# Performance work log

Measured on AMD Instinct MI355X. Metric: run time of the kernel, lower is better.

## Reference

```python
import jax, jax.numpy as jnp
import numpy as np

N_NODES = 50000
N_EDGES = 1_600_000
F_IN = 256
F_OUT = 256


def _gcn_conv(x, edge_index, W, b, num_nodes):
    """PyG GCNConv: add self-loops, symmetric deg^-1/2 normalization,
    linear transform, scatter-add aggregation, plus bias."""
    src, dst = edge_index[0], edge_index[1]
    loop = jnp.arange(num_nodes, dtype=src.dtype)
    src = jnp.concatenate([src, loop])  # [E+N]
    dst = jnp.concatenate([dst, loop])
    # degree of target nodes (edge_weight = 1), computed with self-loops
    deg = jax.ops.segment_sum(jnp.ones_like(dst, dtype=x.dtype), dst,
                              num_segments=num_nodes)
    dis = jnp.where(deg > 0, jax.lax.rsqrt(jnp.maximum(deg, 1.0)), 0.0)
    norm = dis[src] * dis[dst]  # [E+N]
    h = x @ W                   # [N, F_out]
    msg = h[src] * norm[:, None]                      # gather + scale
    out = jax.ops.segment_sum(msg, dst, num_segments=num_nodes)  # scatter-add
    return out + b


def setup_inputs() -> dict:
    key = jax.random.key(0)
    ks = jax.random.split(key, 6)
    x = jax.random.normal(ks[0], (N_NODES, F_IN), dtype=jnp.float32)
    edge_index = jax.random.randint(ks[1], (2, N_EDGES), 0, N_NODES,
                                    dtype=jnp.int64 if jax.config.jax_enable_x64 else jnp.int32)
    s = 1.0 / np.sqrt(F_IN)
    W1 = jax.random.normal(ks[2], (F_IN, F_OUT), dtype=jnp.float32) * s
    b1 = jnp.zeros((F_OUT,), dtype=jnp.float32)
    W2 = jax.random.normal(ks[3], (F_OUT, F_OUT), dtype=jnp.float32) * (1.0 / np.sqrt(F_OUT))
    b2 = jnp.zeros((F_OUT,), dtype=jnp.float32)
    prelu_a = jnp.full((F_OUT,), 0.25, dtype=jnp.float32)  # torch PReLU init
    return {"x": x, "edge_index": edge_index, "W1": W1, "b1": b1,
            "W2": W2, "b2": b2, "prelu_a": prelu_a}


def reference(x, edge_index, W1, b1, W2, b2, prelu_a):
    n = x.shape[0]
    z = _gcn_conv(x, edge_index, W1, b1, n)
    z = _gcn_conv(z, edge_index, W2, b2, n)
    # per-channel PReLU
    z = jnp.where(z >= 0, z, prelu_a[None, :] * z)
    return z
```

## Files before the change

kernel.cpp:

```cpp
#include <hip/hip_runtime.h>
#include <stdint.h>

typedef __attribute__((ext_vector_type(8))) short bf16x8;
typedef __attribute__((ext_vector_type(4))) float f32x4;
typedef __attribute__((ext_vector_type(4))) float float4v;
typedef __attribute__((ext_vector_type(4))) unsigned int u32x4;

#define F 256
#define NCHUNK 8
#define CW 32
#define BKT_SHIFT 7
#define BKT_NODES 128
#define MAXNB 512
#define CAP 6144
#define CHUNK 2048

static __device__ __forceinline__ float asf(uint32_t u) {
  union { uint32_t u; float f; } x; x.u = u; return x.f;
}
static __device__ __forceinline__ unsigned short f2bf(float f) {
  union { float f; uint32_t u; } x; x.f = f;
  uint32_t u = x.u;
  return (unsigned short)((u + 0x7FFFu + ((u >> 16) & 1u)) >> 16);
}

__global__ __launch_bounds__(256) void scatter_kernel(const int* __restrict__ src,
                                                      const int* __restrict__ dst,
                                                      int* __restrict__ gcursor,
                                                      uint32_t* __restrict__ pairs, int E, int NB) {
  __shared__ int cnt[MAXNB];
  __shared__ int gbase[MAXNB];
  const int tid = threadIdx.x;
  for (int t = tid; t < MAXNB; t += 256) cnt[t] = 0;
  __syncthreads();
  const int base = blockIdx.x * CHUNK;
  uint32_t val[8];
  int bk[8], pos[8];
  if (base + CHUNK <= E) {
    const int i0 = base + tid * 8;
    const u32x4 s0 = *reinterpret_cast<const u32x4*>(src + i0);
    const u32x4 s1 = *reinterpret_cast<const u32x4*>(src + i0 + 4);
    const u32x4 d0 = *reinterpret_cast<const u32x4*>(dst + i0);
    const u32x4 d1 = *reinterpret_cast<const u32x4*>(dst + i0 + 4);
    uint32_t sv[8] = {s0.x, s0.y, s0.z, s0.w, s1.x, s1.y, s1.z, s1.w};
    uint32_t dv[8] = {d0.x, d0.y, d0.z, d0.w, d1.x, d1.y, d1.z, d1.w};
#pragma unroll
    for (int j = 0; j < 8; ++j) {
      bk[j] = (int)(dv[j] >> BKT_SHIFT);
      val[j] = sv[j] | ((dv[j] & (BKT_NODES - 1)) << 16);
      pos[j] = atomicAdd(&cnt[bk[j]], 1);
    }
  } else {
#pragma unroll
    for (int j = 0; j < 8; ++j) {
      int i = base + tid * 8 + j;
      if (i < E) {
        uint32_t s = (uint32_t)src[i], d = (uint32_t)dst[i];
        bk[j] = (int)(d >> BKT_SHIFT);
        val[j] = s | ((d & (BKT_NODES - 1)) << 16);
        pos[j] = atomicAdd(&cnt[bk[j]], 1);
      } else bk[j] = -1;
    }
  }
  __syncthreads();
  for (int t = tid; t < NB; t += 256)
    gbase[t] = cnt[t] ? atomicAdd(&gcursor[t], cnt[t]) : 0;
  __syncthreads();
#pragma unroll
  for (int j = 0; j < 8; ++j)
    if (bk[j] >= 0) pairs[(size_t)bk[j] * CAP + gbase[bk[j]] + pos[j]] = val[j];
}

__global__ __launch_bounds__(256) void build_kernel(const uint32_t* __restrict__ pairs,
                                                    const int* __restrict__ gcursor,
                                                    int* __restrict__ row_start,
                                                    int* __restrict__ degv,
                                                    float* __restrict__ dis,
                                                    unsigned short* __restrict__ col, int N) {
  __shared__ int hcnt[BKT_NODES], hcur[BKT_NODES], hend[BKT_NODES];
  __shared__ int s[BKT_NODES];
  const int b = blockIdx.x;
  const int tid = threadIdx.x;
  const int e0 = b * CAP;
  const int e1 = e0 + gcursor[b];
  if (tid < BKT_NODES) hcnt[tid] = 0;
  __syncthreads();
  for (int i = e0 + tid; i < e1; i += 256) atomicAdd(&hcnt[pairs[i] >> 16], 1);
  __syncthreads();
  int v = 0, v8 = 0;
  if (tid < BKT_NODES) { v = hcnt[tid]; v8 = (v + 7) & ~7; s[tid] = v8; }
  __syncthreads();
  for (int off = 1; off < BKT_NODES; off <<= 1) {
    int t = 0;
    if (tid < BKT_NODES && tid >= off) t = s[tid - off];
    __syncthreads();
    if (tid < BKT_NODES) s[tid] += t;
    __syncthreads();
  }
  if (tid < BKT_NODES) {
    const int st = e0 + s[tid] - v8;
    hcur[tid] = st;
    hend[tid] = st + v8;
    const int node = b * BKT_NODES + tid;
    if (node < N) {
      row_start[node] = st;
      degv[node] = v;
      dis[node] = rsqrtf((float)(v + 1));
    }
  }
  __syncthreads();
  for (int i = e0 + tid; i < e1; i += 256) {
    uint32_t pv = pairs[i];
    int p = atomicAdd(&hcur[pv >> 16], 1);
    col[p] = (unsigned short)(pv & 0xFFFFu);
  }
  __syncthreads();
  if (tid < BKT_NODES) {
    for (int p = hcur[tid]; p < hend[tid]; ++p) col[p] = (unsigned short)N;
  }
}

__global__ __launch_bounds__(256) void prep_kernel(const float* __restrict__ W1,
                                                   const float* __restrict__ W2,
                                                   const float* __restrict__ b1,
                                                   unsigned short* __restrict__ W1B,
                                                   unsigned short* __restrict__ W2T,
                                                   float* __restrict__ cv,
                                                   unsigned short* __restrict__ g,
                                                   unsigned short* __restrict__ t,
                                                   float* __restrict__ dis, int N, int NR) {
  const int b = blockIdx.x, tid = threadIdx.x;
  if (b < 256) {
    int i = b * 256 + tid;
    W1B[i] = f2bf(W1[i]);
  } else if (b < 512) {
    int i = (b - 256) * 256 + tid;
    W2T[i] = f2bf(W2[(i & 255) * 256 + (i >> 8)]);
  } else if (b < 768) {
    __shared__ float s[256];
    const int j = b - 512;
    s[tid] = b1[tid] * W2[tid * F + j];
    __syncthreads();
    for (int off = 128; off > 0; off >>= 1) {
      if (tid < off) s[tid] += s[tid + off];
      __syncthreads();
    }
    if (tid == 0) cv[j] = s[0];
  } else {
    const int c = tid >> 5, f = tid & 31;
    g[((size_t)c * NR + N) * CW + f] = 0;
    t[((size_t)c * NR + N) * CW + f] = 0;
    if (tid == 0) dis[N] = 0.f;
  }
}

__global__ __launch_bounds__(256) void rsum_kernel(const float* __restrict__ dis,
                                                   const int* __restrict__ row_start,
                                                   const int* __restrict__ degv,
                                                   const unsigned short* __restrict__ col,
                                                   float* __restrict__ rv, int N) {
  const int n = blockIdx.x * 256 + threadIdx.x;
  if (n >= N) return;
  const int s = row_start[n];
  const int ntr = (degv[n] + 7) >> 3;
  float sum = dis[n];
  for (int t = 0; t < ntr; ++t) {
    const u32x4 cv = *reinterpret_cast<const u32x4*>(col + s + t * 8);
    sum += dis[cv.x & 0xFFFFu] + dis[cv.x >> 16] + dis[cv.y & 0xFFFFu] + dis[cv.y >> 16]
         + dis[cv.z & 0xFFFFu] + dis[cv.z >> 16] + dis[cv.w & 0xFFFFu] + dis[cv.w >> 16];
  }
  rv[n] = dis[n] * sum;
}

template <int A_FP32, int PLAIN>
__global__ __launch_bounds__(256) void gemm_kernel(
    const void* __restrict__ Av,
    const unsigned short* __restrict__ BT,
    const float* __restrict__ dis,
    unsigned short* __restrict__ G, int M, int NR)
{
  const int tid = threadIdx.x;
  const int w = tid >> 6;
  const int l = tid & 63;
  const int row0 = blockIdx.x * 128 + (w >> 1) * 64;
  const int col0 = blockIdx.y * 128 + (w & 1) * 64;
  const int lr = l & 15;
  const int lk = (l >> 4) * 8;

  f32x4 acc[4][4] = {};
  for (int kk = 0; kk < F; kk += 32) {
    bf16x8 a[4], b[4];
#pragma unroll
    for (int i = 0; i < 4; ++i) {
      int r = row0 + i * 16 + lr;
      r = r < M ? r : M - 1;
      if constexpr (A_FP32) {
        const float* A = (const float*)Av;
        const float4v* pA = reinterpret_cast<const float4v*>(A + (size_t)r * F + kk + lk);
        float4v u0 = pA[0], u1 = pA[1];
        bf16x8 af;
        af[0] = (short)f2bf(u0[0]); af[1] = (short)f2bf(u0[1]);
        af[2] = (short)f2bf(u0[2]); af[3] = (short)f2bf(u0[3]);
        af[4] = (short)f2bf(u1[0]); af[5] = (short)f2bf(u1[1]);
        af[6] = (short)f2bf(u1[2]); af[7] = (short)f2bf(u1[3]);
        a[i] = af;
      } else {
        const unsigned short* A = (const unsigned short*)Av;
        a[i] = *reinterpret_cast<const bf16x8*>(A + (size_t)r * F + kk + lk);
      }
      b[i] = *reinterpret_cast<const bf16x8*>(BT + (size_t)(col0 + i * 16 + lr) * F + kk + lk);
    }
#pragma unroll
    for (int i = 0; i < 4; ++i)
#pragma unroll
      for (int j = 0; j < 4; ++j)
        acc[i][j] = __builtin_amdgcn_mfma_f32_16x16x32_bf16(a[i], b[j], acc[i][j], 0, 0, 0);
  }
  const int orow = (l >> 4) * 4;
  const int ocol = l & 15;
#pragma unroll
  for (int i = 0; i < 4; ++i) {
#pragma unroll
    for (int r = 0; r < 4; ++r) {
      int row = row0 + i * 16 + orow + r;
      if (row < M) {
        if constexpr (PLAIN) {
#pragma unroll
          for (int j = 0; j < 4; ++j)
            G[(size_t)row * F + col0 + j * 16 + ocol] = f2bf(acc[i][j][r]);
        } else {
          float d = dis[row];
#pragma unroll
          for (int j = 0; j < 4; ++j) {
            int c = (col0 >> 5) + (j >> 1);
            int f = ((j & 1) << 4) + ocol;
            G[((size_t)c * NR + row) * CW + f] = f2bf(acc[i][j][r] * d);
          }
        }
      }
    }
  }
}

template <int LAST>
__global__ __launch_bounds__(256) void aggregate_kernel(
    const unsigned short* __restrict__ Gc, const float* __restrict__ dis,
    const int* __restrict__ row_start, const int* __restrict__ degv,
    const unsigned short* __restrict__ col,
    const float* __restrict__ bias, const float* __restrict__ pa,
    const float* __restrict__ rv, const float* __restrict__ cvec,
    void* __restrict__ outv, int N, int NR)
{
  const int c   = blockIdx.x & 7;
  const int cb  = blockIdx.x >> 3;
  const int wv  = threadIdx.x >> 6;
  const int l   = threadIdx.x & 63;
  const int grp = l >> 2;
  const int f8  = (l & 3) * 8;
  const unsigned short* __restrict__ base = Gc + (size_t)c * NR * CW + f8;
  const int fb = c * CW + f8;
  float bv[8], qv[8], cvv[8];
  if constexpr (LAST) {
    const float4v* bp = reinterpret_cast<const float4v*>(bias + fb);
    const float4v* qp = reinterpret_cast<const float4v*>(pa + fb);
    const float4v* cp = reinterpret_cast<const float4v*>(cvec + fb);
    float4v b0 = bp[0], b1 = bp[1], q0 = qp[0], q1 = qp[1], c0 = cp[0], c1 = cp[1];
#pragma unroll
    for (int i = 0; i < 4; ++i) {
      bv[i] = b0[i]; bv[4 + i] = b1[i];
      qv[i] = q0[i]; qv[4 + i] = q1[i];
      cvv[i] = c0[i]; cvv[4 + i] = c1[i];
    }
  }

  for (int n0 = cb * 64 + wv * 16; n0 < N; n0 += 256 * 64) {
    const int n = n0 + grp;
    if (n >= N) continue;
    float a0, a1, a2, a3, a4, a5, a6, a7;
    {
      const u32x4 v = *reinterpret_cast<const u32x4*>(base + (size_t)n * CW);
      a0 = asf(v.x << 16); a1 = asf(v.x & 0xFFFF0000u);
      a2 = asf(v.y << 16); a3 = asf(v.y & 0xFFFF0000u);
      a4 = asf(v.z << 16); a5 = asf(v.z & 0xFFFF0000u);
      a6 = asf(v.w << 16); a7 = asf(v.w & 0xFFFF0000u);
    }
    const int s = row_start[n];
    const int ntr = (degv[n] + 7) >> 3;
    for (int tI = 0; tI < ntr; ++tI) {
      const u32x4 cv = *reinterpret_cast<const u32x4*>(col + s + tI * 8);
      const u32x4 g0 = *reinterpret_cast<const u32x4*>(base + (size_t)(cv.x & 0xFFFFu) * CW);
      const u32x4 g1 = *reinterpret_cast<const u32x4*>(base + (size_t)(cv.x >> 16) * CW);
      const u32x4 g2 = *reinterpret_cast<const u32x4*>(base + (size_t)(cv.y & 0xFFFFu) * CW);
      const u32x4 g3 = *reinterpret_cast<const u32x4*>(base + (size_t)(cv.y >> 16) * CW);
      const u32x4 g4 = *reinterpret_cast<const u32x4*>(base + (size_t)(cv.z & 0xFFFFu) * CW);
      const u32x4 g5 = *reinterpret_cast<const u32x4*>(base + (size_t)(cv.z >> 16) * CW);
      const u32x4 g6 = *reinterpret_cast<const u32x4*>(base + (size_t)(cv.w & 0xFFFFu) * CW);
      const u32x4 g7 = *reinterpret_cast<const u32x4*>(base + (size_t)(cv.w >> 16) * CW);
#define ACC8(g) \
      a0 += asf(g.x << 16); a1 += asf(g.x & 0xFFFF0000u); \
      a2 += asf(g.y << 16); a3 += asf(g.y & 0xFFFF0000u); \
      a4 += asf(g.z << 16); a5 += asf(g.z & 0xFFFF0000u); \
      a6 += asf(g.w << 16); a7 += asf(g.w & 0xFFFF0000u);
      ACC8(g0) ACC8(g1) ACC8(g2) ACC8(g3) ACC8(g4) ACC8(g5) ACC8(g6) ACC8(g7)
#undef ACC8
    }
    const float d = dis[n];
    if constexpr (LAST) {
      const float rn = rv[n];
      float r[8] = {a0, a1, a2, a3, a4, a5, a6, a7};
      float4v o0, o1;
#pragma unroll
      for (int i = 0; i < 8; ++i) {
        float ri = fmaf(r[i], d, fmaf(rn, cvv[i], bv[i]));
        ri = fmaxf(ri, 0.f) + qv[i] * fminf(ri, 0.f);
        if (i < 4) o0[i] = ri; else o1[i - 4] = ri;
      }
      float* op = (float*)outv + (size_t)n * F + fb;
      __builtin_nontemporal_store(o0, reinterpret_cast<float4v*>(op));
      __builtin_nontemporal_store(o1, reinterpret_cast<float4v*>(op + 4));
    } else {
      const float dd = d * d;
      u32x4 o;
      o.x = (uint32_t)f2bf(a0 * dd) | ((uint32_t)f2bf(a1 * dd) << 16);
      o.y = (uint32_t)f2bf(a2 * dd) | ((uint32_t)f2bf(a3 * dd) << 16);
      o.z = (uint32_t)f2bf(a4 * dd) | ((uint32_t)f2bf(a5 * dd) << 16);
      o.w = (uint32_t)f2bf(a6 * dd) | ((uint32_t)f2bf(a7 * dd) << 16);
      __builtin_nontemporal_store(o, reinterpret_cast<u32x4*>(
          (unsigned short*)outv + ((size_t)c * NR + n) * CW + f8));
    }
  }
}

extern "C" void kernel_launch(void* const* d_in, const int* in_sizes, int n_in,
                              void* d_out, int out_size, void* d_ws, size_t ws_size,
                              hipStream_t stream) {
  const float* x  = (const float*)d_in[0];
  const int* ei   = (const int*)d_in[1];
  const float* W1 = (const float*)d_in[2];
  const float* b1 = (const float*)d_in[3];
  const float* W2 = (const float*)d_in[4];
  const float* b2 = (const float*)d_in[5];
  const float* pa = (const float*)d_in[6];

  const int N = in_sizes[0] / F;
  const int E = in_sizes[1] / 2;
  const int NR = N + 1;
  const int NB = (N + BKT_NODES - 1) >> BKT_SHIFT;
  const int* src  = ei;
  const int* dstv = ei + E;

  char* p = (char*)d_ws;
  auto alloc = [&](size_t bytes) -> char* {
    char* r = p; p += (bytes + 255) & ~(size_t)255; return r;
  };
  int*   gcursor     = (int*)alloc(sizeof(int) * MAXNB);
  int*   row_start   = (int*)alloc(sizeof(int) * (size_t)N);
  int*   degv        = (int*)alloc(sizeof(int) * (size_t)N);
  float* dis         = (float*)alloc(sizeof(float) * (size_t)(N + 1));
  float* rv          = (float*)alloc(sizeof(float) * (size_t)N);
  float* cv          = (float*)alloc(sizeof(float) * F);
  unsigned short* col = (unsigned short*)alloc(sizeof(short) * (size_t)NB * CAP);
  unsigned short* W1B  = (unsigned short*)alloc(sizeof(short) * F * F);
  unsigned short* W2T  = (unsigned short*)alloc(sizeof(short) * F * F);
  unsigned short* W12T = (unsigned short*)alloc(sizeof(short) * F * F);
  unsigned short* g   = (unsigned short*)alloc(sizeof(short) * (size_t)NR * F);
  unsigned short* t   = (unsigned short*)alloc(sizeof(short) * (size_t)NR * F);
  uint32_t* pairs = (uint32_t*)g;

  hipMemsetAsync(gcursor, 0, sizeof(int) * MAXNB, stream);
  scatter_kernel<<<(E + CHUNK - 1) / CHUNK, 256, 0, stream>>>(src, dstv, gcursor, pairs, E, NB);
  build_kernel<<<NB, 256, 0, stream>>>(pairs, gcursor, row_start, degv, dis, col, N);
  prep_kernel<<<769, 256, 0, stream>>>(W1, W2, b1, W1B, W2T, cv, g, t, dis, N, NR);
  {
    dim3 wgrid(2, 2);
    gemm_kernel<0, 1><<<wgrid, 256, 0, stream>>>((const void*)W2T, W1B, nullptr, W12T, F, 0);
  }
  rsum_kernel<<<(N + 255) / 256, 256, 0, stream>>>(dis, row_start, degv, col, rv, N);

  dim3 ggrid((N + 127) / 128, F / 128);
  gemm_kernel<1, 0><<<ggrid, 256, 0, stream>>>((const void*)x, W12T, dis, g, N, NR);
  aggregate_kernel<0><<<2048, 256, 0, stream>>>(g, dis, row_start, degv, col,
                                                nullptr, nullptr, nullptr, nullptr, t, N, NR);
  aggregate_kernel<1><<<2048, 256, 0, stream>>>(t, dis, row_start, degv, col,
                                                b2, pa, rv, cv, d_out, N, NR);
}
```

Baseline: 270.9 us.

## Fuse rsum into prep, widen GEMM tiles to full width, double scatter chunk

The rsum kernel becomes extra blocks of prep_kernel, which removes one launch. The GEMM now has each block compute a 128x256 output tile with 8 column subtiles per wave, instead of a 2D grid of 128x128 tiles. That lets the A rows (fp32 x, converted to bf16) be read and converted once instead of twice, at the cost of more accumulator registers and lower occupancy (launch bounds min 1 block). The scatter kernel now handles 4096 edges per block instead of 2048, which halves the number of global atomics on the bucket cursors.

```diff
diff --git a/kernel.cpp b/kernel.cpp
--- a/kernel.cpp
+++ b/kernel.cpp
@@ -13,7 +13,7 @@
 #define BKT_NODES 128
 #define MAXNB 512
 #define CAP 6144
-#define CHUNK 2048
+#define CHUNK 4096
 
 static __device__ __forceinline__ float asf(uint32_t u) {
   union { uint32_t u; float f; } x; x.u = u; return x.f;
@@ -34,26 +34,28 @@
   for (int t = tid; t < MAXNB; t += 256) cnt[t] = 0;
   __syncthreads();
   const int base = blockIdx.x * CHUNK;
-  uint32_t val[8];
-  int bk[8], pos[8];
+  uint32_t val[16];
+  int bk[16], pos[16];
   if (base + CHUNK <= E) {
-    const int i0 = base + tid * 8;
-    const u32x4 s0 = *reinterpret_cast<const u32x4*>(src + i0);
-    const u32x4 s1 = *reinterpret_cast<const u32x4*>(src + i0 + 4);
-    const u32x4 d0 = *reinterpret_cast<const u32x4*>(dst + i0);
-    const u32x4 d1 = *reinterpret_cast<const u32x4*>(dst + i0 + 4);
-    uint32_t sv[8] = {s0.x, s0.y, s0.z, s0.w, s1.x, s1.y, s1.z, s1.w};
-    uint32_t dv[8] = {d0.x, d0.y, d0.z, d0.w, d1.x, d1.y, d1.z, d1.w};
-#pragma unroll
-    for (int j = 0; j < 8; ++j) {
-      bk[j] = (int)(dv[j] >> BKT_SHIFT);
-      val[j] = sv[j] | ((dv[j] & (BKT_NODES - 1)) << 16);
-      pos[j] = atomicAdd(&cnt[bk[j]], 1);
+    const int i0 = base + tid * 16;
+#pragma unroll
+    for (int q = 0; q < 4; ++q) {
+      const u32x4 s0 = *reinterpret_cast<const u32x4*>(src + i0 + q * 4);
+      const u32x4 d0 = *reinterpret_cast<const u32x4*>(dst + i0 + q * 4);
+      uint32_t sv[4] = {s0.x, s0.y, s0.z, s0.w};
+      uint32_t dv[4] = {d0.x, d0.y, d0.z, d0.w};
+#pragma unroll
+      for (int j = 0; j < 4; ++j) {
+        int jj = q * 4 + j;
+        bk[jj] = (int)(dv[j] >> BKT_SHIFT);
+        val[jj] = sv[j] | ((dv[j] & (BKT_NODES - 1)) << 16);
+        pos[jj] = atomicAdd(&cnt[bk[jj]], 1);
+      }
     }
   } else {
 #pragma unroll
-    for (int j = 0; j < 8; ++j) {
-      int i = base + tid * 8 + j;
+    for (int j = 0; j < 16; ++j) {
+      int i = base + tid * 16 + j;
       if (i < E) {
         uint32_t s = (uint32_t)src[i], d = (uint32_t)dst[i];
         bk[j] = (int)(d >> BKT_SHIFT);
@@ -67,7 +69,7 @@
     gbase[t] = cnt[t] ? atomicAdd(&gcursor[t], cnt[t]) : 0;
   __syncthreads();
 #pragma unroll
-  for (int j = 0; j < 8; ++j)
+  for (int j = 0; j < 16; ++j)
     if (bk[j] >= 0) pairs[(size_t)bk[j] * CAP + gbase[bk[j]] + pos[j]] = val[j];
 }
 
@@ -128,7 +130,12 @@
                                                    float* __restrict__ cv,
                                                    unsigned short* __restrict__ g,
                                                    unsigned short* __restrict__ t,
-                                                   float* __restrict__ dis, int N, int NR) {
+                                                   float* __restrict__ dis,
+                                                   const int* __restrict__ row_start,
+                                                   const int* __restrict__ degv,
+                                                   const unsigned short* __restrict__ col,
+                                                   float* __restrict__ rv,
+                                                   int N, int NR) {
   const int b = blockIdx.x, tid = threadIdx.x;
   if (b < 256) {
     int i = b * 256 + tid;
@@ -146,34 +153,29 @@
       __syncthreads();
     }
     if (tid == 0) cv[j] = s[0];
-  } else {
+  } else if (b == 768) {
     const int c = tid >> 5, f = tid & 31;
     g[((size_t)c * NR + N) * CW + f] = 0;
     t[((size_t)c * NR + N) * CW + f] = 0;
     if (tid == 0) dis[N] = 0.f;
-  }
-}
-
-__global__ __launch_bounds__(256) void rsum_kernel(const float* __restrict__ dis,
-                                                   const int* __restrict__ row_start,
-                                                   const int* __restrict__ degv,
-                                                   const unsigned short* __restrict__ col,
-                                                   float* __restrict__ rv, int N) {
-  const int n = blockIdx.x * 256 + threadIdx.x;
-  if (n >= N) return;
-  const int s = row_start[n];
-  const int ntr = (degv[n] + 7) >> 3;
-  float sum = dis[n];
-  for (int t = 0; t < ntr; ++t) {
-    const u32x4 cv = *reinterpret_cast<const u32x4*>(col + s + t * 8);
-    sum += dis[cv.x & 0xFFFFu] + dis[cv.x >> 16] + dis[cv.y & 0xFFFFu] + dis[cv.y >> 16]
-         + dis[cv.z & 0xFFFFu] + dis[cv.z >> 16] + dis[cv.w & 0xFFFFu] + dis[cv.w >> 16];
-  }
-  rv[n] = dis[n] * sum;
+  } else {
+    const int n = (b - 769) * 256 + tid;
+    if (n < N) {
+      const int s0 = row_start[n];
+      const int ntr = (degv[n] + 7) >> 3;
+      float sum = dis[n];
+      for (int tI = 0; tI < ntr; ++tI) {
+        const u32x4 cvv = *reinterpret_cast<const u32x4*>(col + s0 + tI * 8);
+        sum += dis[cvv.x & 0xFFFFu] + dis[cvv.x >> 16] + dis[cvv.y & 0xFFFFu] + dis[cvv.y >> 16]
+             + dis[cvv.z & 0xFFFFu] + dis[cvv.z >> 16] + dis[cvv.w & 0xFFFFu] + dis[cvv.w >> 16];
+      }
+      rv[n] = dis[n] * sum;
+    }
+  }
 }
 
 template <int A_FP32, int PLAIN>
-__global__ __launch_bounds__(256) void gemm_kernel(
+__global__ __launch_bounds__(256, 1) void gemm_kernel(
     const void* __restrict__ Av,
     const unsigned short* __restrict__ BT,
     const float* __restrict__ dis,
@@ -183,13 +185,13 @@
   const int w = tid >> 6;
   const int l = tid & 63;
   const int row0 = blockIdx.x * 128 + (w >> 1) * 64;
-  const int col0 = blockIdx.y * 128 + (w & 1) * 64;
+  const int col0 = (w & 1) * 128;
   const int lr = l & 15;
   const int lk = (l >> 4) * 8;
 
-  f32x4 acc[4][4] = {};
+  f32x4 acc[4][8] = {};
   for (int kk = 0; kk < F; kk += 32) {
-    bf16x8 a[4], b[4];
+    bf16x8 a[4], b[8];
 #pragma unroll
     for (int i = 0; i < 4; ++i) {
       int r = row0 + i * 16 + lr;
@@ -208,12 +210,14 @@
         const unsigned short* A = (const unsigned short*)Av;
         a[i] = *reinterpret_cast<const bf16x8*>(A + (size_t)r * F + kk + lk);
       }
-      b[i] = *reinterpret_cast<const bf16x8*>(BT + (size_t)(col0 + i * 16 + lr) * F + kk + lk);
-    }
+    }
+#pragma unroll
+    for (int j = 0; j < 8; ++j)
+      b[j] = *reinterpret_cast<const bf16x8*>(BT + (size_t)(col0 + j * 16 + lr) * F + kk + lk);
 #pragma unroll
     for (int i = 0; i < 4; ++i)
 #pragma unroll
-      for (int j = 0; j < 4; ++j)
+      for (int j = 0; j < 8; ++j)
         acc[i][j] = __builtin_amdgcn_mfma_f32_16x16x32_bf16(a[i], b[j], acc[i][j], 0, 0, 0);
   }
   const int orow = (l >> 4) * 4;
@@ -226,12 +230,12 @@
       if (row < M) {
         if constexpr (PLAIN) {
 #pragma unroll
-          for (int j = 0; j < 4; ++j)
+          for (int j = 0; j < 8; ++j)
             G[(size_t)row * F + col0 + j * 16 + ocol] = f2bf(acc[i][j][r]);
         } else {
           float d = dis[row];
 #pragma unroll
-          for (int j = 0; j < 4; ++j) {
+          for (int j = 0; j < 8; ++j) {
             int c = (col0 >> 5) + (j >> 1);
             int f = ((j & 1) << 4) + ocol;
             G[((size_t)c * NR + row) * CW + f] = f2bf(acc[i][j][r] * d);
@@ -370,15 +374,11 @@
   hipMemsetAsync(gcursor, 0, sizeof(int) * MAXNB, stream);
   scatter_kernel<<<(E + CHUNK - 1) / CHUNK, 256, 0, stream>>>(src, dstv, gcursor, pairs, E, NB);
   build_kernel<<<NB, 256, 0, stream>>>(pairs, gcursor, row_start, degv, dis, col, N);
-  prep_kernel<<<769, 256, 0, stream>>>(W1, W2, b1, W1B, W2T, cv, g, t, dis, N, NR);
-  {
-    dim3 wgrid(2, 2);
-    gemm_kernel<0, 1><<<wgrid, 256, 0, stream>>>((const void*)W2T, W1B, nullptr, W12T, F, 0);
-  }
-  rsum_kernel<<<(N + 255) / 256, 256, 0, stream>>>(dis, row_start, degv, col, rv, N);
-
-  dim3 ggrid((N + 127) / 128, F / 128);
-  gemm_kernel<1, 0><<<ggrid, 256, 0, stream>>>((const void*)x, W12T, dis, g, N, NR);
+  prep_kernel<<<769 + (N + 255) / 256, 256, 0, stream>>>(W1, W2, b1, W1B, W2T, cv, g, t, dis,
+                                                         row_start, degv, col, rv, N, NR);
+  gemm_kernel<0, 1><<<2, 256, 0, stream>>>((const void*)W2T, W1B, nullptr, W12T, F, 0);
+
+  gemm_kernel<1, 0><<<(N + 127) / 128, 256, 0, stream>>>((const void*)x, W12T, dis, g, N, NR);
   aggregate_kernel<0><<<2048, 256, 0, stream>>>(g, dis, row_start, degv, col,
                                                 nullptr, nullptr, nullptr, nullptr, t, N, NR);
   aggregate_kernel<1><<<2048, 256, 0, stream>>>(t, dis, row_start, degv, col,
```

Measured after the change: 255.2 us (median of 2 runs). 5.8% less time.
